# Kernel optimization log

Measured on AMD Instinct MI355X. Metric: run time of the kernel, lower is better.

## Reference

```python
import jax, jax.numpy as jnp
import numpy as np

N_FEAT = 1024
N_HEAD = 8
CONTEXT_SIZES = [21, 41]
HPS = N_HEAD // len(CONTEXT_SIZES)  # heads per scale = 4


def setup_inputs() -> dict:
    key = jax.random.key(0)
    ks = jax.random.split(key, 9)
    B, T, D = 4, 1024, N_FEAT
    s = 1.0 / np.sqrt(D)
    return {
        "query": jax.random.normal(ks[0], (B, T, D), dtype=jnp.float32),
        "key": jax.random.normal(ks[1], (B, T, D), dtype=jnp.float32),
        "value": jax.random.normal(ks[2], (B, T, D), dtype=jnp.float32),
        # weights stored [in, out] (torch Linear applies x @ W.T)
        "W_qv": jax.random.normal(ks[3], (D, 2 * D), dtype=jnp.float32) * s,
        "W2_0": jax.random.normal(ks[4], (D, HPS * CONTEXT_SIZES[0]), dtype=jnp.float32) * s,
        "W2_1": jax.random.normal(ks[5], (D, HPS * CONTEXT_SIZES[1]), dtype=jnp.float32) * s,
        "scale_weights": jnp.ones((len(CONTEXT_SIZES),), dtype=jnp.float32) / len(CONTEXT_SIZES),
        "W_out": jax.random.normal(ks[6], (D, D), dtype=jnp.float32) * s,
    }


def _sliding_window(v, c):
    # v: [B, T, D] -> [B, T, c, D], symmetric zero pad of (c-1)//2 each side
    B, T, D = v.shape
    half = (c - 1) // 2
    v_pad = jnp.pad(v, ((0, 0), (half, half), (0, 0)))
    idx = jnp.arange(T)[:, None] + jnp.arange(c)[None, :]  # [T, c]
    return v_pad[:, idx]  # [B, T, c, D]


def reference(query, key, value, W_qv, W2_0, W2_1, scale_weights, W_out):
    B, T, D = query.shape
    qv = query @ W_qv                      # [B, T, 2D]
    q, v = jnp.split(qv, 2, axis=-1)       # each [B, T, D]
    sw = jax.nn.softmax(scale_weights)     # [n_scales]
    head_dim = D // HPS
    x = jnp.zeros_like(query)
    for i, (c, W2) in enumerate(zip(CONTEXT_SIZES, [W2_0, W2_1])):
        # synthesized attention logits: [B, T, HPS, c]
        logits = (jax.nn.relu(q) @ W2).reshape(B, T, HPS, c)
        attn = jax.nn.softmax(logits, axis=-1)
        vw = _sliding_window(v, c).reshape(B, T, c, HPS, head_dim)
        out = jnp.einsum('bthc,btchd->bthd', attn, vw).reshape(B, T, D)
        x = x + sw[i] * out
    return x @ W_out
```

## Files before the change

### kernel.cpp

```cpp
#include <hip/hip_runtime.h>
#include <hip/hip_bf16.h>
#include <math.h>

#define BB 4
#define TT 1024
#define DD 1024
#define HPS 4
#define C0 21
#define C1 41
#define N0 (HPS * C0)
#define N1 (HPS * C1)
#define NL 256
#define BT (BB * TT)
#define KSPLIT 4
#define TB2 32
#define HALO 20
#define HB2 (TB2 + 2 * HALO)

typedef unsigned int uint;
typedef __bf16 bf16x8 __attribute__((ext_vector_type(8)));
typedef float f32x4 __attribute__((ext_vector_type(4)));

__device__ __forceinline__ ushort f2bf(float f) {
    union { float f; uint u; } v; v.f = f;
    uint u = v.u;
    uint r = (u + 0x7FFFu + ((u >> 16) & 1u)) >> 16;
    return (ushort)r;
}
__device__ __forceinline__ float bf2f(ushort s) {
    union { uint u; float f; } v; v.u = ((uint)s) << 16;
    return v.f;
}

#define RQ  4096
#define R1  (RQ + 2048)
#define R2  (R1 + 1024)
#define R3  (R2 + 96)
#define R4  (R3 + 192)

__device__ __forceinline__ void transpose_tile(
    const float* __restrict__ in, ushort* __restrict__ out,
    int K, int Nin, int n_base, int Npad, int nx, int ky, int tid)
{
    __shared__ float tile[32][33];
    const int tx = tid & 31;
    const int ty = tid >> 5;
    const int n0 = nx * 32;
    const int k0 = ky * 32;
    #pragma unroll
    for (int i = 0; i < 4; i++) {
        int k = k0 + ty + i * 8;
        int n = n0 + tx;
        float v = (k < K && n < Nin) ? in[(size_t)k * Nin + n] : 0.0f;
        tile[ty + i * 8][tx] = v;
    }
    __syncthreads();
    #pragma unroll
    for (int i = 0; i < 4; i++) {
        int n = n0 + ty + i * 8;
        int k = k0 + tx;
        if (n < Npad && k < K)
            out[(size_t)(n_base + n) * K + k] = f2bf(tile[tx][ty + i * 8]);
    }
}

__global__ __launch_bounds__(256) void convert_all(
    const float* __restrict__ query, ushort* __restrict__ query_bf,
    const float* __restrict__ W_qv,  ushort* __restrict__ WqvT,
    const float* __restrict__ W_out, ushort* __restrict__ WoutT,
    const float* __restrict__ W2_0, const float* __restrict__ W2_1,
    ushort* __restrict__ W2T)
{
    const int blk = blockIdx.x;
    const int tid = threadIdx.x;
    if (blk < RQ) {
        int i = blk * 1024 + tid * 4;
        float4 v = *(const float4*)(query + i);
        ushort4 o;
        o.x = f2bf(v.x); o.y = f2bf(v.y); o.z = f2bf(v.z); o.w = f2bf(v.w);
        *(ushort4*)(query_bf + i) = o;
    } else if (blk < R1) {
        int idx = blk - RQ;
        transpose_tile(W_qv, WqvT, DD, 2 * DD, 0, 2 * DD, idx & 63, idx >> 6, tid);
    } else if (blk < R2) {
        int idx = blk - R1;
        transpose_tile(W_out, WoutT, DD, DD, 0, DD, idx & 31, idx >> 5, tid);
    } else if (blk < R3) {
        int idx = blk - R2;
        transpose_tile(W2_0, W2T, DD, N0, 0, N0, idx % 3, idx / 3, tid);
    } else {
        int idx = blk - R3;
        transpose_tile(W2_1, W2T, DD, N1, N0, NL - N0, idx % 6, idx / 6, tid);
    }
}

__device__ __forceinline__ int xcd_chunk(int blk, int nblk) {
    return (blk & 7) * (nblk >> 3) + (blk >> 3);
}

template<int NT>
__global__ __launch_bounds__(512, 4) void gemm_mfma(
    const ushort* __restrict__ A, const ushort* __restrict__ Bt,
    int K, int klen,
    float* __restrict__ Cf, ushort* __restrict__ Cb, ushort* __restrict__ Cv,
    int mode, int ldc)
{
    constexpr int MT = 128;
    constexpr int MR = 4;
    constexpr int NR = NT / 64;
    __shared__ ushort As[2][MT * 64];
    __shared__ ushort Bs[2][NT * 64];

    const int tid = threadIdx.x;
    const int wv  = tid >> 6;
    const int ln  = tid & 63;

    const int ntile = gridDim.x * gridDim.y;
    const int tile  = xcd_chunk(blockIdx.y * gridDim.x + blockIdx.x, ntile);
    const int bx = tile % gridDim.x;
    const int by = tile / gridDim.x;
    const int row0 = by * MT;
    const int col0 = bx * NT;
    const int kbase = blockIdx.z * klen;

    const int wr = (wv >> 2) * 64;
    const int wc = (wv & 3) * (NT / 4);
    const int l15 = ln & 15;
    const int lq  = ln >> 4;

    f32x4 acc[MR][NR];
    #pragma unroll
    for (int i = 0; i < MR; i++)
        #pragma unroll
        for (int j = 0; j < NR; j++)
            acc[i][j] = (f32x4){0.f, 0.f, 0.f, 0.f};

    const int rsub = ln >> 3;
    const int cg   = (ln & 7) ^ rsub;
    const ushort* gA = A  + (size_t)(row0 + wv * 8 + rsub) * K + kbase + cg * 8;
    const ushort* gB = Bt + (size_t)(col0 + wv * 8 + rsub) * K + kbase + cg * 8;
    const int fx = l15 & 7;
    const int nt = klen / 64;

    auto STAGE = [&](int buf, int kk) {
        #pragma unroll
        for (int i = 0; i < 2; i++) {
            __builtin_amdgcn_global_load_lds(
                (const __attribute__((address_space(1))) void*)(gA + (size_t)i * 64 * K + kk),
                (__attribute__((address_space(3))) void*)(&As[buf][(i * 64 + wv * 8) * 64]),
                16, 0, 0);
        }
        #pragma unroll
        for (int i = 0; i < NT / 64; i++) {
            __builtin_amdgcn_global_load_lds(
                (const __attribute__((address_space(1))) void*)(gB + (size_t)i * 64 * K + kk),
                (__attribute__((address_space(3))) void*)(&Bs[buf][(i * 64 + wv * 8) * 64]),
                16, 0, 0);
        }
    };

    auto COMPUTE = [&](int buf) {
        #pragma unroll
        for (int s = 0; s < 2; s++) {
            const int ca = ((s * 4 + lq) ^ fx) * 8;
            bf16x8 af[MR], bfr[NR];
            #pragma unroll
            for (int mi = 0; mi < MR; mi++)
                af[mi] = *(const bf16x8*)&As[buf][(wr + mi * 16 + l15) * 64 + ca];
            #pragma unroll
            for (int ni = 0; ni < NR; ni++)
                bfr[ni] = *(const bf16x8*)&Bs[buf][(wc + ni * 16 + l15) * 64 + ca];
            #pragma unroll
            for (int mi = 0; mi < MR; mi++)
                #pragma unroll
                for (int ni = 0; ni < NR; ni++)
                    acc[mi][ni] = __builtin_amdgcn_mfma_f32_16x16x32_bf16(
                        af[mi], bfr[ni], acc[mi][ni], 0, 0, 0);
        }
    };

    int cur = 0;
    STAGE(0, 0);
    __syncthreads();
    for (int t = 0; t < nt; ++t) {
        const bool more = (t + 1 < nt);
        if (more) STAGE(cur ^ 1, (t + 1) * 64);
        COMPUTE(cur);
        if (more) __syncthreads();
        cur ^= 1;
    }

    #pragma unroll
    for (int mi = 0; mi < MR; mi++) {
        #pragma unroll
        for (int ni = 0; ni < NR; ni++) {
            #pragma unroll
            for (int r = 0; r < 4; r++) {
                int row = row0 + wr + mi * 16 + lq * 4 + r;
                int col = col0 + wc + ni * 16 + l15;
                float v = acc[mi][ni][r];
                if (mode == 0) {
                    Cf[(size_t)row * ldc + col] = v;
                } else if (mode == 2) {
                    if (col < DD) Cb[(size_t)row * DD + col] = f2bf(fmaxf(v, 0.0f));
                    else          Cv[(size_t)row * DD + (col - DD)] = f2bf(v);
                } else {
                    Cf[((size_t)blockIdx.z * BT + row) * ldc + col] = v;
                }
            }
        }
    }
}

__global__ __launch_bounds__(256) void attn_window_kernel(
    const ushort* __restrict__ v,
    const float* __restrict__ Lp,
    const float* __restrict__ scale_w,
    ushort* __restrict__ x)
{
    __shared__ ushort vs[HB2][256];
    __shared__ float  cw[TB2][42];

    const int blk = blockIdx.x;
    const int h  = blk & 3;
    const int tt = (blk >> 2) & 31;
    const int b  = blk >> 7;
    const int t0 = tt * TB2;
    const int tid = threadIdx.x;
    const size_t PS = (size_t)BT * NL;

    const ushort* vb = v + (size_t)b * TT * DD + h * 256;
    #pragma unroll
    for (int i = 0; i < 9; i++) {
        int c = i * 256 + tid;
        int r = c >> 5;
        int cir = c & 31;
        int t = t0 - HALO + r;
        uint4 val = make_uint4(0, 0, 0, 0);
        if (t >= 0 && t < TT)
            val = *(const uint4*)(vb + (size_t)t * DD + cir * 8);
        *(uint4*)(&vs[r][cir * 8]) = val;
    }

    if (tid < TB2) {
        const int bt = b * TT + t0 + tid;
        const float* Lb = Lp + (size_t)bt * NL;

        float s0 = scale_w[0], s1 = scale_w[1];
        float mm = fmaxf(s0, s1);
        float e0 = __expf(s0 - mm), e1 = __expf(s1 - mm);
        float inv01 = 1.0f / (e0 + e1);
        float sw0 = e0 * inv01, sw1 = e1 * inv01;

        float w0[C0], w1[C1];
        {
            const int off = h * C0;
            float m = -1e30f;
            #pragma unroll
            for (int j = 0; j < C0; j++) {
                float sacc = 0.0f;
                #pragma unroll
                for (int z = 0; z < KSPLIT; z++) sacc += Lb[(size_t)z * PS + off + j];
                w0[j] = sacc;
                m = fmaxf(m, w0[j]);
            }
            float s = 0.0f;
            #pragma unroll
            for (int j = 0; j < C0; j++) { w0[j] = __expf(w0[j] - m); s += w0[j]; }
            float inv = sw0 / s;
            #pragma unroll
            for (int j = 0; j < C0; j++) w0[j] *= inv;
        }
        {
            const int off = N0 + h * C1;
            float m = -1e30f;
            #pragma unroll
            for (int j = 0; j < C1; j++) {
                float sacc = 0.0f;
                #pragma unroll
                for (int z = 0; z < KSPLIT; z++) sacc += Lb[(size_t)z * PS + off + j];
                w1[j] = sacc;
                m = fmaxf(m, w1[j]);
            }
            float s = 0.0f;
            #pragma unroll
            for (int j = 0; j < C1; j++) { w1[j] = __expf(w1[j] - m); s += w1[j]; }
            float inv = sw1 / s;
            #pragma unroll
            for (int j = 0; j < C1; j++) w1[j] *= inv;
        }
        #pragma unroll
        for (int o = 0; o < C1; o++) {
            float w = w1[o];
            if (o >= 10 && o <= 30) w += w0[o - 10];
            cw[tid][o] = w;
        }
    }
    __syncthreads();

    const int tq = tid >> 6;
    const int dg = tid & 63;
    const int d  = dg * 4;

    for (int tloc = 0; tloc < 8; tloc++) {
        const int tp = tq * 8 + tloc;
        f32x4 acc = {0.f, 0.f, 0.f, 0.f};
        #pragma unroll
        for (int o = 0; o < C1; o++) {
            float w = cw[tp][o];
            ushort4 vv = *(const ushort4*)(&vs[tp + o][d]);
            acc[0] = fmaf(w, bf2f(vv.x), acc[0]);
            acc[1] = fmaf(w, bf2f(vv.y), acc[1]);
            acc[2] = fmaf(w, bf2f(vv.z), acc[2]);
            acc[3] = fmaf(w, bf2f(vv.w), acc[3]);
        }
        const int bt = b * TT + t0 + tp;
        ushort4 o4;
        o4.x = f2bf(acc[0]); o4.y = f2bf(acc[1]);
        o4.z = f2bf(acc[2]); o4.w = f2bf(acc[3]);
        *(ushort4*)(x + (size_t)bt * DD + h * 256 + d) = o4;
    }
}

extern "C" void kernel_launch(void* const* d_in, const int* in_sizes, int n_in,
                              void* d_out, int out_size, void* d_ws, size_t ws_size,
                              hipStream_t stream)
{
    const float* query   = (const float*)d_in[0];
    const float* W_qv    = (const float*)d_in[3];
    const float* W2_0    = (const float*)d_in[4];
    const float* W2_1    = (const float*)d_in[5];
    const float* scale_w = (const float*)d_in[6];
    const float* W_out   = (const float*)d_in[7];
    float* out = (float*)d_out;

    char* ws = (char*)d_ws;
    ushort* W2T      = (ushort*)ws;                 ws += (size_t)NL * DD * 2;
    ushort* WoutT    = (ushort*)ws;                 ws += (size_t)DD * DD * 2;
    ushort* query_bf = (ushort*)ws;                 ws += (size_t)BT * DD * 2;
    ushort* WqvT     = (ushort*)ws;                 ws += (size_t)2 * DD * DD * 2;
    ushort* reluq    = (ushort*)ws;                 ws += (size_t)BT * DD * 2;
    ushort* vbuf     = (ushort*)ws;                 ws += (size_t)BT * DD * 2;
    ushort* xbuf     = (ushort*)ws;                 ws += (size_t)BT * DD * 2;
    float*  logitsP  = (float*)ws;                  ws += (size_t)KSPLIT * BT * NL * 4;

    convert_all<<<R4, 256, 0, stream>>>(query, query_bf, W_qv, WqvT,
                                        W_out, WoutT, W2_0, W2_1, W2T);

    {   dim3 grid(2 * DD / 128, BT / 128, 1);
        gemm_mfma<128><<<grid, 512, 0, stream>>>(query_bf, WqvT, DD, DD,
                                                 nullptr, reluq, vbuf, 2, 0); }
    {   dim3 grid(NL / 64, BT / 128, KSPLIT);
        gemm_mfma<64><<<grid, 512, 0, stream>>>(reluq, W2T, DD, DD / KSPLIT,
                                                logitsP, nullptr, nullptr, 3, NL); }
    attn_window_kernel<<<512, 256, 0, stream>>>(vbuf, logitsP, scale_w, xbuf);

    {   dim3 grid(DD / 64, BT / 128, 1);
        gemm_mfma<64><<<grid, 512, 0, stream>>>(xbuf, WoutT, DD, DD,
                                                out, nullptr, nullptr, 0, DD); }
}
```

Baseline: 177.3 us.

## Fuse logits GEMM into windowed attention kernel with per-head W2 layout

Removes the separate split-K logits GEMM and its fp32 partial-sum buffer. The attention-window kernel now computes each block's 32x64 logits tile for its head directly with MFMA, staging reluq and a per-head padded W2 layout into LDS via global_load_lds. W2 is rearranged so each head's 21+41 columns sit together in a 64-row slab. This saves a launch and the round trip of writing and re-reading the partial logits, but each block now runs a serial K=1024 loop that only 512 blocks share, and reluq rows are re-read once per head.

```diff
diff --git a/kernel.cpp b/kernel.cpp
--- a/kernel.cpp
+++ b/kernel.cpp
@@ -10,9 +10,7 @@
 #define C1 41
 #define N0 (HPS * C0)
 #define N1 (HPS * C1)
-#define NL 256
 #define BT (BB * TT)
-#define KSPLIT 4
 #define TB2 32
 #define HALO 20
 #define HB2 (TB2 + 2 * HALO)
@@ -40,7 +38,7 @@
 
 __device__ __forceinline__ void transpose_tile(
     const float* __restrict__ in, ushort* __restrict__ out,
-    int K, int Nin, int n_base, int Npad, int nx, int ky, int tid)
+    int K, int Nin, int nx, int ky, int tid, int hs, int roff)
 {
     __shared__ float tile[32][33];
     const int tx = tid & 31;
@@ -59,8 +57,10 @@
     for (int i = 0; i < 4; i++) {
         int n = n0 + ty + i * 8;
         int k = k0 + tx;
-        if (n < Npad && k < K)
-            out[(size_t)(n_base + n) * K + k] = f2bf(tile[tx][ty + i * 8]);
+        if (n < Nin && k < K) {
+            int row = (n / hs) * 64 + roff + (n % hs);
+            out[(size_t)row * K + k] = f2bf(tile[tx][ty + i * 8]);
+        }
     }
 }
 
@@ -69,7 +69,7 @@
     const float* __restrict__ W_qv,  ushort* __restrict__ WqvT,
     const float* __restrict__ W_out, ushort* __restrict__ WoutT,
     const float* __restrict__ W2_0, const float* __restrict__ W2_1,
-    ushort* __restrict__ W2T)
+    ushort* __restrict__ W2Tph)
 {
     const int blk = blockIdx.x;
     const int tid = threadIdx.x;
@@ -81,16 +81,16 @@
         *(ushort4*)(query_bf + i) = o;
     } else if (blk < R1) {
         int idx = blk - RQ;
-        transpose_tile(W_qv, WqvT, DD, 2 * DD, 0, 2 * DD, idx & 63, idx >> 6, tid);
+        transpose_tile(W_qv, WqvT, DD, 2 * DD, idx & 63, idx >> 6, tid, 2 * DD, 0);
     } else if (blk < R2) {
         int idx = blk - R1;
-        transpose_tile(W_out, WoutT, DD, DD, 0, DD, idx & 31, idx >> 5, tid);
+        transpose_tile(W_out, WoutT, DD, DD, idx & 31, idx >> 5, tid, DD, 0);
     } else if (blk < R3) {
         int idx = blk - R2;
-        transpose_tile(W2_0, W2T, DD, N0, 0, N0, idx % 3, idx / 3, tid);
+        transpose_tile(W2_0, W2Tph, DD, N0, idx % 3, idx / 3, tid, C0, 0);
     } else {
         int idx = blk - R3;
-        transpose_tile(W2_1, W2T, DD, N1, N0, NL - N0, idx % 6, idx / 6, tid);
+        transpose_tile(W2_1, W2Tph, DD, N1, idx % 6, idx / 6, tid, C1, C0);
     }
 }
 
@@ -201,25 +201,35 @@
                 float v = acc[mi][ni][r];
                 if (mode == 0) {
                     Cf[(size_t)row * ldc + col] = v;
-                } else if (mode == 2) {
+                } else {
                     if (col < DD) Cb[(size_t)row * DD + col] = f2bf(fmaxf(v, 0.0f));
                     else          Cv[(size_t)row * DD + (col - DD)] = f2bf(v);
-                } else {
-                    Cf[((size_t)blockIdx.z * BT + row) * ldc + col] = v;
                 }
             }
         }
     }
 }
 
-__global__ __launch_bounds__(256) void attn_window_kernel(
+#define LOFF_VS 0
+#define LOFF_QS (LOFF_VS + HB2 * 256 * 2)
+#define LOFF_WS (LOFF_QS + 2 * TB2 * 64 * 2)
+#define LOFF_LS (LOFF_WS + 2 * 64 * 64 * 2)
+#define LOFF_CW (LOFF_LS + TB2 * 65 * 4)
+#define LDS_TOTAL (LOFF_CW + TB2 * 42 * 4)
+
+__global__ __launch_bounds__(256) void attn_fused_kernel(
+    const ushort* __restrict__ reluq,
+    const ushort* __restrict__ W2Tph,
     const ushort* __restrict__ v,
-    const float* __restrict__ Lp,
     const float* __restrict__ scale_w,
     ushort* __restrict__ x)
 {
-    __shared__ ushort vs[HB2][256];
-    __shared__ float  cw[TB2][42];
+    extern __shared__ __attribute__((aligned(16))) char smem[];
+    ushort (*vs)[256] = (ushort (*)[256])(smem + LOFF_VS);
+    ushort* qs = (ushort*)(smem + LOFF_QS);
+    ushort* ws2 = (ushort*)(smem + LOFF_WS);
+    float  (*Ls)[65] = (float (*)[65])(smem + LOFF_LS);
+    float  (*cw)[42] = (float (*)[42])(smem + LOFF_CW);
 
     const int blk = blockIdx.x;
     const int h  = blk & 3;
@@ -227,7 +237,7 @@
     const int b  = blk >> 7;
     const int t0 = tt * TB2;
     const int tid = threadIdx.x;
-    const size_t PS = (size_t)BT * NL;
+    const int bt0 = b * TT + t0;
 
     const ushort* vb = v + (size_t)b * TT * DD + h * 256;
     #pragma unroll
@@ -242,10 +252,67 @@
         *(uint4*)(&vs[r][cir * 8]) = val;
     }
 
+    const int wv = tid >> 6;
+    const int ln = tid & 63;
+    const int wr = (wv >> 1) * 16;
+    const int wc = (wv & 1) * 32;
+    const int l15 = ln & 15;
+    const int lq  = ln >> 4;
+    const int rsub = ln >> 3;
+    const int cg   = (ln & 7) ^ rsub;
+    const int fx = l15 & 7;
+
+    const ushort* gA = reluq + (size_t)(bt0 + wv * 8 + rsub) * DD + cg * 8;
+    const ushort* gB = W2Tph + ((size_t)h * 64 + wv * 16 + rsub) * DD + cg * 8;
+
+    f32x4 acc[2];
+    acc[0] = (f32x4){0.f, 0.f, 0.f, 0.f};
+    acc[1] = (f32x4){0.f, 0.f, 0.f, 0.f};
+
+    auto STAGEQ = [&](int buf, int kk) {
+        __builtin_amdgcn_global_load_lds(
+            (const __attribute__((address_space(1))) void*)(gA + kk),
+            (__attribute__((address_space(3))) void*)(&qs[(size_t)buf * TB2 * 64 + (wv * 8) * 64]),
+            16, 0, 0);
+        #pragma unroll
+        for (int i = 0; i < 2; i++) {
+            __builtin_amdgcn_global_load_lds(
+                (const __attribute__((address_space(1))) void*)(gB + (size_t)i * 8 * DD + kk),
+                (__attribute__((address_space(3))) void*)(&ws2[(size_t)buf * 64 * 64 + (wv * 16 + i * 8) * 64]),
+                16, 0, 0);
+        }
+    };
+    auto COMPQ = [&](int buf) {
+        #pragma unroll
+        for (int s = 0; s < 2; s++) {
+            const int ca = ((s * 4 + lq) ^ fx) * 8;
+            bf16x8 a = *(const bf16x8*)&qs[(size_t)buf * TB2 * 64 + (wr + l15) * 64 + ca];
+            #pragma unroll
+            for (int ni = 0; ni < 2; ni++) {
+                bf16x8 bb = *(const bf16x8*)&ws2[(size_t)buf * 64 * 64 + (wc + ni * 16 + l15) * 64 + ca];
+                acc[ni] = __builtin_amdgcn_mfma_f32_16x16x32_bf16(a, bb, acc[ni], 0, 0, 0);
+            }
+        }
+    };
+
+    int cur = 0;
+    STAGEQ(0, 0);
+    __syncthreads();
+    for (int t = 0; t < 16; ++t) {
+        const bool more = (t + 1 < 16);
+        if (more) STAGEQ(cur ^ 1, (t + 1) * 64);
+        COMPQ(cur);
+        if (more) __syncthreads();
+        cur ^= 1;
+    }
+    #pragma unroll
+    for (int ni = 0; ni < 2; ni++)
+        #pragma unroll
+        for (int r = 0; r < 4; r++)
+            Ls[wr + lq * 4 + r][wc + ni * 16 + l15] = acc[ni][r];
+    __syncthreads();
+
     if (tid < TB2) {
-        const int bt = b * TT + t0 + tid;
-        const float* Lb = Lp + (size_t)bt * NL;
-
         float s0 = scale_w[0], s1 = scale_w[1];
         float mm = fmaxf(s0, s1);
         float e0 = __expf(s0 - mm), e1 = __expf(s1 - mm);
@@ -254,16 +321,9 @@
 
         float w0[C0], w1[C1];
         {
-            const int off = h * C0;
             float m = -1e30f;
             #pragma unroll
-            for (int j = 0; j < C0; j++) {
-                float sacc = 0.0f;
-                #pragma unroll
-                for (int z = 0; z < KSPLIT; z++) sacc += Lb[(size_t)z * PS + off + j];
-                w0[j] = sacc;
-                m = fmaxf(m, w0[j]);
-            }
+            for (int j = 0; j < C0; j++) { w0[j] = Ls[tid][j]; m = fmaxf(m, w0[j]); }
             float s = 0.0f;
             #pragma unroll
             for (int j = 0; j < C0; j++) { w0[j] = __expf(w0[j] - m); s += w0[j]; }
@@ -272,16 +332,9 @@
             for (int j = 0; j < C0; j++) w0[j] *= inv;
         }
         {
-            const int off = N0 + h * C1;
             float m = -1e30f;
             #pragma unroll
-            for (int j = 0; j < C1; j++) {
-                float sacc = 0.0f;
-                #pragma unroll
-                for (int z = 0; z < KSPLIT; z++) sacc += Lb[(size_t)z * PS + off + j];
-                w1[j] = sacc;
-                m = fmaxf(m, w1[j]);
-            }
+            for (int j = 0; j < C1; j++) { w1[j] = Ls[tid][C0 + j]; m = fmaxf(m, w1[j]); }
             float s = 0.0f;
             #pragma unroll
             for (int j = 0; j < C1; j++) { w1[j] = __expf(w1[j] - m); s += w1[j]; }
@@ -304,20 +357,20 @@
 
     for (int tloc = 0; tloc < 8; tloc++) {
         const int tp = tq * 8 + tloc;
-        f32x4 acc = {0.f, 0.f, 0.f, 0.f};
+        f32x4 o4acc = {0.f, 0.f, 0.f, 0.f};
         #pragma unroll
         for (int o = 0; o < C1; o++) {
             float w = cw[tp][o];
             ushort4 vv = *(const ushort4*)(&vs[tp + o][d]);
-            acc[0] = fmaf(w, bf2f(vv.x), acc[0]);
-            acc[1] = fmaf(w, bf2f(vv.y), acc[1]);
-            acc[2] = fmaf(w, bf2f(vv.z), acc[2]);
-            acc[3] = fmaf(w, bf2f(vv.w), acc[3]);
-        }
-        const int bt = b * TT + t0 + tp;
+            o4acc[0] = fmaf(w, bf2f(vv.x), o4acc[0]);
+            o4acc[1] = fmaf(w, bf2f(vv.y), o4acc[1]);
+            o4acc[2] = fmaf(w, bf2f(vv.z), o4acc[2]);
+            o4acc[3] = fmaf(w, bf2f(vv.w), o4acc[3]);
+        }
+        const int bt = bt0 + tp;
         ushort4 o4;
-        o4.x = f2bf(acc[0]); o4.y = f2bf(acc[1]);
-        o4.z = f2bf(acc[2]); o4.w = f2bf(acc[3]);
+        o4.x = f2bf(o4acc[0]); o4.y = f2bf(o4acc[1]);
+        o4.z = f2bf(o4acc[2]); o4.w = f2bf(o4acc[3]);
         *(ushort4*)(x + (size_t)bt * DD + h * 256 + d) = o4;
     }
 }
@@ -335,25 +388,22 @@
     float* out = (float*)d_out;
 
     char* ws = (char*)d_ws;
-    ushort* W2T      = (ushort*)ws;                 ws += (size_t)NL * DD * 2;
+    ushort* W2Tph    = (ushort*)ws;                 ws += (size_t)4 * 64 * DD * 2;
     ushort* WoutT    = (ushort*)ws;                 ws += (size_t)DD * DD * 2;
     ushort* query_bf = (ushort*)ws;                 ws += (size_t)BT * DD * 2;
     ushort* WqvT     = (ushort*)ws;                 ws += (size_t)2 * DD * DD * 2;
     ushort* reluq    = (ushort*)ws;                 ws += (size_t)BT * DD * 2;
     ushort* vbuf     = (ushort*)ws;                 ws += (size_t)BT * DD * 2;
     ushort* xbuf     = (ushort*)ws;                 ws += (size_t)BT * DD * 2;
-    float*  logitsP  = (float*)ws;                  ws += (size_t)KSPLIT * BT * NL * 4;
 
     convert_all<<<R4, 256, 0, stream>>>(query, query_bf, W_qv, WqvT,
-                                        W_out, WoutT, W2_0, W2_1, W2T);
+                                        W_out, WoutT, W2_0, W2_1, W2Tph);
 
     {   dim3 grid(2 * DD / 128, BT / 128, 1);
         gemm_mfma<128><<<grid, 512, 0, stream>>>(query_bf, WqvT, DD, DD,
                                                  nullptr, reluq, vbuf, 2, 0); }
-    {   dim3 grid(NL / 64, BT / 128, KSPLIT);
-        gemm_mfma<64><<<grid, 512, 0, stream>>>(reluq, W2T, DD, DD / KSPLIT,
-                                                logitsP, nullptr, nullptr, 3, NL); }
-    attn_window_kernel<<<512, 256, 0, stream>>>(vbuf, logitsP, scale_w, xbuf);
+    attn_fused_kernel<<<512, 256, LDS_TOTAL, stream>>>(reluq, W2Tph, vbuf,
+                                                       scale_w, xbuf);
 
     {   dim3 grid(DD / 64, BT / 128, 1);
         gemm_mfma<64><<<grid, 512, 0, stream>>>(xbuf, WoutT, DD, DD,
```

Result: faster. 168.1 us (-5.2%).
